# Performance work log

Measured on AMD Instinct MI355X. Metric: run time of the kernel, lower is better.

## Reference

```python
import jax, jax.numpy as jnp
import numpy as np

N_NODES = 100000
N_EDGES = 1250000
IN_DIM = 12
HID = 64
N_LAYERS = 3
LN_EPS = 1e-5
LEAKY_SLOPE = 0.01


def _layer_norm(x, g, b):
    mu = jnp.mean(x, axis=-1, keepdims=True)
    var = jnp.var(x, axis=-1, keepdims=True)
    return (x - mu) * jax.lax.rsqrt(var + LN_EPS) * g + b


def setup_inputs() -> dict:
    key = jax.random.key(0)
    ks = jax.random.split(key, 16)
    s = 0.1  # param init scale
    return {
        "x": jax.random.normal(ks[0], (N_NODES, IN_DIM), jnp.float32),
        "edge_index": jax.random.randint(ks[1], (2, N_EDGES), 0, N_NODES, jnp.int64),
        "edge_weight": jax.random.uniform(ks[2], (N_EDGES,), jnp.float32),
        "in_W": s * jax.random.normal(ks[3], (IN_DIM, HID), jnp.float32),
        "in_b": jnp.zeros((HID,), jnp.float32),
        "lin_W": s * jax.random.normal(ks[4], (N_LAYERS, HID, HID), jnp.float32),
        "lin_b": jnp.zeros((N_LAYERS, HID), jnp.float32),
        "att_W": s * jax.random.normal(ks[5], (N_LAYERS, 2 * HID, 1), jnp.float32),
        "att_b": jnp.zeros((N_LAYERS, 1), jnp.float32),
        "ln_g": jnp.ones((N_LAYERS, HID), jnp.float32),
        "ln_b": jnp.zeros((N_LAYERS, HID), jnp.float32),
        "out1_W": s * jax.random.normal(ks[6], (HID, HID // 2), jnp.float32),
        "out1_b": jnp.zeros((HID // 2,), jnp.float32),
        "out2_W": s * jax.random.normal(ks[7], (HID // 2, 1), jnp.float32),
        "out2_b": jnp.zeros((1,), jnp.float32),
    }


def reference(x, edge_index, edge_weight, in_W, in_b, lin_W, lin_b,
              att_W, att_b, ln_g, ln_b, out1_W, out1_b, out2_W, out2_b):
    row, col = edge_index[0], edge_index[1]
    h = x @ in_W + in_b  # [N, HID]
    for i in range(N_LAYERS):
        hl = h @ lin_W[i] + lin_b[i]  # [N, HID]
        h_i = hl[row]  # [E, HID]
        h_j = hl[col]  # [E, HID]
        att_in = jnp.concatenate([h_i, h_j], axis=-1)  # [E, 2*HID]
        scores = jax.nn.leaky_relu(att_in @ att_W[i] + att_b[i], LEAKY_SLOPE)  # [E, 1]
        scores = jax.nn.softmax(scores, axis=0)  # global softmax over edges (as in source)
        scores = scores * edge_weight[:, None]
        messages = scores * h_j  # [E, HID]
        agg = jax.ops.segment_sum(messages, row, num_segments=N_NODES)
        h_new = jax.nn.relu(hl + agg)
        h_new = _layer_norm(h_new, ln_g[i], ln_b[i])
        # dropout is identity in eval mode
        h = h + h_new
    z = jax.nn.relu(h @ out1_W + out1_b)
    return jax.nn.sigmoid(z @ out2_W + out2_b)  # [N, 1]
```

## Files before the change

### kernel.cpp

```cpp
#include <hip/hip_runtime.h>
#include <hip/hip_fp8.h>
#include <math.h>

#define N_NODES 100000
#define N_EDGES 1250000
#define IN_DIM 12
#define HID 64
#define N_LAYERS 3
#define LN_EPS 1e-5f
#define SLOPE 0.01f

#define NODE_BLOCKS ((N_NODES + 3) / 4)
#define EDGE_TBLOCKS ((N_EDGES + 255) / 256)
#define MFMA_BLOCKS2 ((N_NODES + 127) / 128)
#define OUT_BLOCKS ((N_NODES + 63) / 64)
#define NEDGE_BLOCKS ((N_NODES + 255) / 256)

#define BUCKETS 256
#define BUCKET_NODES 391
#define P1_EDGES 4096
#define P1_BLOCKS ((N_EDGES + P1_EDGES - 1) / P1_EDGES)

#define LEW_SCALE 2048.0f
#define LEW_INV (1.0f / 2048.0f)

typedef short bf16x8 __attribute__((ext_vector_type(8)));
typedef float f32x4 __attribute__((ext_vector_type(4)));
typedef float f32x2 __attribute__((ext_vector_type(2)));

#if defined(__has_builtin)
#if __has_builtin(__builtin_amdgcn_cvt_pk_f32_fp8)
#define HAVE_PK_FP8 1
#endif
#endif

static __device__ __forceinline__ unsigned short f2bf(float f) {
  union { float f; unsigned int u; } v; v.f = f;
  unsigned int r = v.u + 0x7FFFu + ((v.u >> 16) & 1u);
  return (unsigned short)(r >> 16);
}
static __device__ __forceinline__ unsigned char f2e4(float f) {
  return __hip_fp8_e4m3(f).__x;
}
static __device__ __forceinline__ float e42f(unsigned char b) {
  __hip_fp8_e4m3 d; d.__x = b;
  return (float)d;
}

__global__ void k_in_proj(const float* __restrict__ x,
                          const float* __restrict__ W,
                          const float* __restrict__ b,
                          float* __restrict__ h) {
  __shared__ float sW[IN_DIM * HID];
  for (int i = threadIdx.x; i < IN_DIM * HID; i += blockDim.x) sW[i] = W[i];
  __syncthreads();
  int wave = threadIdx.x >> 6, lane = threadIdx.x & 63;
  int n = blockIdx.x * 4 + wave;
  if (n >= N_NODES) return;
  float acc = b[lane];
#pragma unroll
  for (int k = 0; k < IN_DIM; ++k)
    acc += x[n * IN_DIM + k] * sW[k * HID + lane];
  h[n * HID + lane] = acc;
}

__global__ void k_bhist(const int* __restrict__ ei, unsigned* __restrict__ bcnt) {
  __shared__ unsigned cnt[BUCKETS];
  int t = threadIdx.x;
  cnt[t] = 0;
  __syncthreads();
  int base = blockIdx.x * P1_EDGES;
#pragma unroll
  for (int i = 0; i < 16; ++i) {
    int e = base + i * 256 + t;
    if (e < N_EDGES) atomicAdd(&cnt[(unsigned)ei[e] / BUCKET_NODES], 1u);
  }
  __syncthreads();
  if (cnt[t]) atomicAdd(&bcnt[t], cnt[t]);
}

__global__ void k_bscan(const unsigned* __restrict__ bcnt,
                        unsigned* __restrict__ boffs,
                        unsigned* __restrict__ gbcur,
                        int* __restrict__ rowptr) {
  __shared__ unsigned sm[BUCKETS];
  int t = threadIdx.x;
  unsigned v = bcnt[t];
  sm[t] = v;
  __syncthreads();
  for (int st = 1; st < BUCKETS; st <<= 1) {
    unsigned tv = (t >= st) ? sm[t - st] : 0u;
    __syncthreads();
    sm[t] += tv;
    __syncthreads();
  }
  unsigned excl = sm[t] - v;
  boffs[t] = excl;
  gbcur[t] = excl;
  if (t == 0) {
    boffs[BUCKETS] = N_EDGES;
    rowptr[N_NODES] = N_EDGES;
  }
}

__global__ void k_fill_p1(const int* __restrict__ ei, const float* __restrict__ ew,
                          unsigned* __restrict__ gbcur,
                          unsigned long long* __restrict__ tmp) {
  __shared__ unsigned cnt[BUCKETS], gbase[BUCKETS], lofs[BUCKETS];
  int t = threadIdx.x;
  cnt[t] = 0;
  __syncthreads();
  int base = blockIdx.x * P1_EDGES;
#pragma unroll
  for (int i = 0; i < 16; ++i) {
    int e = base + i * 256 + t;
    if (e < N_EDGES) atomicAdd(&cnt[(unsigned)ei[e] / BUCKET_NODES], 1u);
  }
  __syncthreads();
  {
    unsigned c = cnt[t];
    gbase[t] = c ? atomicAdd(&gbcur[t], c) : 0u;
    lofs[t] = 0;
  }
  __syncthreads();
#pragma unroll
  for (int i = 0; i < 16; ++i) {
    int e = base + i * 256 + t;
    if (e < N_EDGES) {
      unsigned r = (unsigned)ei[e], c = (unsigned)ei[N_EDGES + e];
      float lew = __logf(ew[e]);
      lew = fmaxf(lew, -15.9995f);
      unsigned q = (unsigned)(-lew * LEW_SCALE + 0.5f);
      if (q > 32767u) q = 32767u;
      unsigned b = r / BUCKET_NODES;
      unsigned idx = atomicAdd(&lofs[b], 1u);
      tmp[gbase[b] + idx] = ((unsigned long long)r << 32)
                          | ((unsigned long long)c << 15) | q;
    }
  }
}

__global__ void k_fill_p2(const unsigned* __restrict__ boffs,
                          const unsigned long long* __restrict__ tmp,
                          int* __restrict__ rowptr,
                          unsigned* __restrict__ packed) {
  __shared__ unsigned lhist[512];
  __shared__ unsigned lcur[512];
  int b = blockIdx.x, t = threadIdx.x;
  int nb0 = b * BUCKET_NODES;
  int nb1 = min(nb0 + BUCKET_NODES, N_NODES);
  int nn = nb1 - nb0;
  int beg = (int)boffs[b];
  int end = (int)boffs[b + 1];

  lhist[t] = 0;
  __syncthreads();
  for (int i = beg + t; i < end; i += 512) {
    int r = (int)(tmp[i] >> 32);
    atomicAdd(&lhist[r - nb0], 1u);
  }
  __syncthreads();
  unsigned degv = lhist[t];
  for (int st = 1; st < 512; st <<= 1) {
    unsigned tv = (t >= st) ? lhist[t - st] : 0u;
    __syncthreads();
    lhist[t] += tv;
    __syncthreads();
  }
  unsigned excl = lhist[t] - degv;
  if (t < nn) rowptr[nb0 + t] = beg + (int)excl;
  lcur[t] = (unsigned)beg + excl;
  __syncthreads();
  for (int i = beg + t; i < end; i += 512) {
    unsigned long long rec = tmp[i];
    int r = (int)(rec >> 32);
    unsigned pos = atomicAdd(&lcur[r - nb0], 1u);
    packed[pos] = (unsigned)(rec & 0xFFFFFFFFu);
  }
}

__global__ void k_prep(const float* __restrict__ lin_W,
                       const float* __restrict__ lin_b,
                       const float* __restrict__ att_W,
                       float* __restrict__ uvec,
                       float* __restrict__ ucst) {
  int l = blockIdx.x, j = threadIdx.x;
  const float* Wl = lin_W + l * HID * HID;
  const float* a1 = att_W + l * 2 * HID;
  const float* a2 = a1 + HID;
  float s1 = 0.f, s2 = 0.f;
  for (int c = 0; c < HID; ++c) {
    float w = Wl[j * HID + c];
    s1 += w * a1[c];
    s2 += w * a2[c];
  }
  uvec[l * 128 + j] = s1;
  uvec[l * 128 + 64 + j] = s2;
  float t1 = lin_b[l * HID + j] * a1[j];
  float t2 = lin_b[l * HID + j] * a2[j];
#pragma unroll
  for (int off = 32; off > 0; off >>= 1) {
    t1 += __shfl_xor(t1, off, 64);
    t2 += __shfl_xor(t2, off, 64);
  }
  if (j == 0) { ucst[l * 2] = t1; ucst[l * 2 + 1] = t2; }
}

__global__ void k_lin_mfma(const float* __restrict__ h,
                           const float* __restrict__ W,
                           const float* __restrict__ bias,
                           const float* __restrict__ uvec,
                           const float* __restrict__ ucst,
                           float* __restrict__ hl,
                           unsigned char* __restrict__ hl8,
                           float* __restrict__ alpha1,
                           float* __restrict__ alpha2) {
  __shared__ unsigned short Wt[HID * 72];
  for (int idx = threadIdx.x; idx < HID * HID; idx += 256) {
    int k = idx >> 6, n = idx & 63;
    Wt[n * 72 + k] = f2bf(W[idx]);
  }
  __syncthreads();

  int wave = threadIdx.x >> 6, lane = threadIdx.x & 63;
  int g = lane >> 4, r = lane & 15;

#pragma unroll
  for (int tile = 0; tile < 2; ++tile) {
    int nb = blockIdx.x * 128 + tile * 64 + wave * 16;
    int row = nb + r;
    bool rowok = row < N_NODES;
    if (nb >= N_NODES) break;

    f32x4 f0 = {0,0,0,0}, f1 = {0,0,0,0}, f2v = {0,0,0,0}, f3 = {0,0,0,0};
    if (rowok) {
      const float* hrow = h + (size_t)row * HID;
      f0  = *(const f32x4*)(hrow + g * 8);
      f1  = *(const f32x4*)(hrow + g * 8 + 4);
      f2v = *(const f32x4*)(hrow + 32 + g * 8);
      f3  = *(const f32x4*)(hrow + 32 + g * 8 + 4);
    }
    bf16x8 a0, a1f;
#pragma unroll
    for (int i = 0; i < 4; ++i) {
      a0[i]      = (short)f2bf(f0[i]);
      a0[i + 4]  = (short)f2bf(f1[i]);
      a1f[i]     = (short)f2bf(f2v[i]);
      a1f[i + 4] = (short)f2bf(f3[i]);
    }

    f32x4 acc[4] = {{0,0,0,0},{0,0,0,0},{0,0,0,0},{0,0,0,0}};
#pragma unroll
    for (int nt = 0; nt < 4; ++nt) {
      bf16x8 b0 = *(const bf16x8*)&Wt[(nt * 16 + r) * 72 + g * 8];
      bf16x8 b1 = *(const bf16x8*)&Wt[(nt * 16 + r) * 72 + 32 + g * 8];
      acc[nt] = __builtin_amdgcn_mfma_f32_16x16x32_bf16(a0, b0, acc[nt], 0, 0, 0);
      acc[nt] = __builtin_amdgcn_mfma_f32_16x16x32_bf16(a1f, b1, acc[nt], 0, 0, 0);
    }

    {
      const float* u1 = uvec;
      const float* u2 = uvec + HID;
      f32x4 ua = *(const f32x4*)(u1 + g * 8),      ub = *(const f32x4*)(u1 + g * 8 + 4);
      f32x4 uc = *(const f32x4*)(u1 + 32 + g * 8), ud = *(const f32x4*)(u1 + 32 + g * 8 + 4);
      float p1 = f0[0]*ua[0]+f0[1]*ua[1]+f0[2]*ua[2]+f0[3]*ua[3]
               + f1[0]*ub[0]+f1[1]*ub[1]+f1[2]*ub[2]+f1[3]*ub[3]
               + f2v[0]*uc[0]+f2v[1]*uc[1]+f2v[2]*uc[2]+f2v[3]*uc[3]
               + f3[0]*ud[0]+f3[1]*ud[1]+f3[2]*ud[2]+f3[3]*ud[3];
      ua = *(const f32x4*)(u2 + g * 8);      ub = *(const f32x4*)(u2 + g * 8 + 4);
      uc = *(const f32x4*)(u2 + 32 + g * 8); ud = *(const f32x4*)(u2 + 32 + g * 8 + 4);
      float p2 = f0[0]*ua[0]+f0[1]*ua[1]+f0[2]*ua[2]+f0[3]*ua[3]
               + f1[0]*ub[0]+f1[1]*ub[1]+f1[2]*ub[2]+f1[3]*ub[3]
               + f2v[0]*uc[0]+f2v[1]*uc[1]+f2v[2]*uc[2]+f2v[3]*uc[3]
               + f3[0]*ud[0]+f3[1]*ud[1]+f3[2]*ud[2]+f3[3]*ud[3];
      p1 += __shfl_xor(p1, 16, 64); p1 += __shfl_xor(p1, 32, 64);
      p2 += __shfl_xor(p2, 16, 64); p2 += __shfl_xor(p2, 32, 64);
      if (g == 0 && rowok) {
        alpha1[row] = p1 + ucst[0];
        alpha2[row] = p2 + ucst[1];
      }
    }

#pragma unroll
    for (int nt = 0; nt < 4; ++nt) {
      float bv = bias[nt * 16 + r];
#pragma unroll
      for (int reg = 0; reg < 4; ++reg) {
        int n2 = nb + g * 4 + reg;
        if (n2 < N_NODES) {
          float v = acc[nt][reg] + bv;
          hl[(size_t)n2 * HID + nt * 16 + r] = v;
          hl8[(size_t)n2 * HID + nt * 16 + r] = f2e4(v);
        }
      }
    }
  }
}

__global__ void k_edge(const int* __restrict__ rowptr,
                       const unsigned* __restrict__ packed,
                       const float* __restrict__ alpha1,
                       const float* __restrict__ alpha2,
                       const float* __restrict__ attB,
                       float* __restrict__ slw,
                       float* __restrict__ pmax,
                       float* __restrict__ psum,
                       int* __restrict__ counter,
                       float* __restrict__ red) {
  int t = threadIdx.x;
  int n = blockIdx.x * 256 + t;
  float m = -INFINITY, sum = 0.f;
  if (n < N_NODES) {
    float a1 = alpha1[n] + attB[0];
    int beg = rowptr[n];
    int end = rowptr[n + 1];
    for (int p = beg; p < end; ++p) {
      unsigned u = packed[p];
      float sc = a1 + alpha2[u >> 15];
      sc = sc > 0.f ? sc : SLOPE * sc;
      slw[p] = sc - (float)(u & 0x7FFFu) * LEW_INV;
      if (sc > m) { sum *= __expf(m - sc); m = sc; }
      sum += __expf(sc - m);
    }
  }
  __shared__ float smax[256], ssum[256];
  __shared__ bool last;
  smax[t] = m; ssum[t] = sum;
  __syncthreads();
  for (int st = 128; st > 0; st >>= 1) {
    if (t < st) {
      float ma = smax[t], mb = smax[t + st];
      float sa = ssum[t], sb = ssum[t + st];
      float mm = fmaxf(ma, mb);
      float ss = 0.f;
      if (mm != -INFINITY)
        ss = (ma == -INFINITY ? 0.f : sa * __expf(ma - mm))
           + (mb == -INFINITY ? 0.f : sb * __expf(mb - mm));
      smax[t] = mm; ssum[t] = ss;
    }
    __syncthreads();
  }
  if (t == 0) {
    pmax[blockIdx.x] = smax[0];
    psum[blockIdx.x] = ssum[0];
    __threadfence();
    int old = atomicAdd(counter, 1);
    last = (old == (int)gridDim.x - 1);
  }
  __syncthreads();
  if (!last) return;
  __threadfence();
  volatile const float* vpm = pmax;
  volatile const float* vps = psum;
  float m2 = -INFINITY, s2 = 0.f;
  for (int i = t; i < (int)gridDim.x; i += 256) {
    float mb = vpm[i], sb = vps[i];
    if (mb != -INFINITY) {
      if (mb > m2) { s2 *= __expf(m2 - mb); m2 = mb; }
      s2 += sb * __expf(mb - m2);
    }
  }
  __syncthreads();
  smax[t] = m2; ssum[t] = s2;
  __syncthreads();
  for (int st = 128; st > 0; st >>= 1) {
    if (t < st) {
      float ma = smax[t], mb = smax[t + st];
      float sa = ssum[t], sb = ssum[t + st];
      float mm = fmaxf(ma, mb);
      float ss = 0.f;
      if (mm != -INFINITY)
        ss = (ma == -INFINITY ? 0.f : sa * __expf(ma - mm))
           + (mb == -INFINITY ? 0.f : sb * __expf(mb - mm));
      smax[t] = mm; ssum[t] = ss;
    }
    __syncthreads();
  }
  if (t == 0) {
    red[0] = smax[0];
    red[1] = ssum[0];
    *counter = 0;
  }
}

__global__ void k_exp2(f32x4* __restrict__ slw, const float* __restrict__ red) {
  int i = blockIdx.x * 256 + threadIdx.x;
  int nvec = (N_EDGES + 3) / 4;
  if (i >= nvec) return;
  float M = red[0];
  f32x4 v = slw[i];
  v[0] = __expf(v[0] - M);
  v[1] = __expf(v[1] - M);
  v[2] = __expf(v[2] - M);
  v[3] = __expf(v[3] - M);
  slw[i] = v;
}

__global__ void k_agg_update(const int* __restrict__ rowptr,
                             const unsigned* __restrict__ packed,
                             const float* __restrict__ w,
                             const float* __restrict__ red,
                             const float* __restrict__ hl,
                             const unsigned char* __restrict__ hl8,
                             const float* __restrict__ gam,
                             const float* __restrict__ bet,
                             float* __restrict__ h) {
  int wave = threadIdx.x >> 6, lane = threadIdx.x & 63;
  int n = blockIdx.x * 4 + wave;
  if (n >= N_NODES) return;
  int g = lane >> 4, q = lane & 15;
  int beg = rowptr[n];
  int end = rowptr[n + 1];

  float a0 = 0.f, a1 = 0.f, a2 = 0.f, a3 = 0.f;
  for (int k = beg; k < end; k += 16) {
    int ke0 = k + g, ke1 = k + 4 + g, ke2 = k + 8 + g, ke3 = k + 12 + g;
    bool v0 = ke0 < end, v1 = ke1 < end, v2 = ke2 < end, v3 = ke3 < end;
    unsigned u0 = packed[v0 ? ke0 : beg];
    unsigned u1 = packed[v1 ? ke1 : beg];
    unsigned u2 = packed[v2 ? ke2 : beg];
    unsigned u3 = packed[v3 ? ke3 : beg];
    float w0 = v0 ? w[ke0] : 0.f;
    float w1 = v1 ? w[ke1] : 0.f;
    float w2 = v2 ? w[ke2] : 0.f;
    float w3 = v3 ? w[ke3] : 0.f;
    unsigned d0 = *(const unsigned*)(hl8 + (size_t)(u0 >> 15) * HID + q * 4);
    unsigned d1 = *(const unsigned*)(hl8 + (size_t)(u1 >> 15) * HID + q * 4);
    unsigned d2 = *(const unsigned*)(hl8 + (size_t)(u2 >> 15) * HID + q * 4);
    unsigned d3 = *(const unsigned*)(hl8 + (size_t)(u3 >> 15) * HID + q * 4);
#ifdef HAVE_PK_FP8
    f32x2 l0 = __builtin_amdgcn_cvt_pk_f32_fp8((int)d0, 0);
    f32x2 h0 = __builtin_amdgcn_cvt_pk_f32_fp8((int)d0, 1);
    f32x2 l1 = __builtin_amdgcn_cvt_pk_f32_fp8((int)d1, 0);
    f32x2 h1 = __builtin_amdgcn_cvt_pk_f32_fp8((int)d1, 1);
    f32x2 l2 = __builtin_amdgcn_cvt_pk_f32_fp8((int)d2, 0);
    f32x2 h2 = __builtin_amdgcn_cvt_pk_f32_fp8((int)d2, 1);
    f32x2 l3 = __builtin_amdgcn_cvt_pk_f32_fp8((int)d3, 0);
    f32x2 h3 = __builtin_amdgcn_cvt_pk_f32_fp8((int)d3, 1);
    a0 += w0 * l0[0] + w1 * l1[0] + w2 * l2[0] + w3 * l3[0];
    a1 += w0 * l0[1] + w1 * l1[1] + w2 * l2[1] + w3 * l3[1];
    a2 += w0 * h0[0] + w1 * h1[0] + w2 * h2[0] + w3 * h3[0];
    a3 += w0 * h0[1] + w1 * h1[1] + w2 * h2[1] + w3 * h3[1];
#else
    a0 += w0 * e42f(d0 & 0xffu) + w1 * e42f(d1 & 0xffu)
        + w2 * e42f(d2 & 0xffu) + w3 * e42f(d3 & 0xffu);
    a1 += w0 * e42f((d0 >> 8) & 0xffu) + w1 * e42f((d1 >> 8) & 0xffu)
        + w2 * e42f((d2 >> 8) & 0xffu) + w3 * e42f((d3 >> 8) & 0xffu);
    a2 += w0 * e42f((d0 >> 16) & 0xffu) + w1 * e42f((d1 >> 16) & 0xffu)
        + w2 * e42f((d2 >> 16) & 0xffu) + w3 * e42f((d3 >> 16) & 0xffu);
    a3 += w0 * e42f(d0 >> 24) + w1 * e42f(d1 >> 24)
        + w2 * e42f(d2 >> 24) + w3 * e42f(d3 >> 24);
#endif
  }
  a0 += __shfl_xor(a0, 16, 64); a0 += __shfl_xor(a0, 32, 64);
  a1 += __shfl_xor(a1, 16, 64); a1 += __shfl_xor(a1, 32, 64);
  a2 += __shfl_xor(a2, 16, 64); a2 += __shfl_xor(a2, 32, 64);
  a3 += __shfl_xor(a3, 16, 64); a3 += __shfl_xor(a3, 32, 64);

  float inv = 1.0f / red[1];
  const float* hlrow = hl + (size_t)n * HID + q * 4;
  float v0 = fmaxf(hlrow[0] + a0 * inv, 0.f);
  float v1 = fmaxf(hlrow[1] + a1 * inv, 0.f);
  float v2 = fmaxf(hlrow[2] + a2 * inv, 0.f);
  float v3 = fmaxf(hlrow[3] + a3 * inv, 0.f);

  float ms = v0 + v1 + v2 + v3;
  ms += __shfl_xor(ms, 1, 64); ms += __shfl_xor(ms, 2, 64);
  ms += __shfl_xor(ms, 4, 64); ms += __shfl_xor(ms, 8, 64);
  float m = ms * (1.0f / HID);
  float d0 = v0 - m, d1 = v1 - m, d2 = v2 - m, d3 = v3 - m;
  float vs = d0 * d0 + d1 * d1 + d2 * d2 + d3 * d3;
  vs += __shfl_xor(vs, 1, 64); vs += __shfl_xor(vs, 2, 64);
  vs += __shfl_xor(vs, 4, 64); vs += __shfl_xor(vs, 8, 64);
  float rs = rsqrtf(vs * (1.0f / HID) + LN_EPS);

  if (g == 0) {
    float* hrow = h + (size_t)n * HID + q * 4;
    f32x4 hv = *(const f32x4*)hrow;
    f32x4 gv = *(const f32x4*)(gam + q * 4);
    f32x4 bv = *(const f32x4*)(bet + q * 4);
    f32x4 o;
    o[0] = hv[0] + d0 * rs * gv[0] + bv[0];
    o[1] = hv[1] + d1 * rs * gv[1] + bv[1];
    o[2] = hv[2] + d2 * rs * gv[2] + bv[2];
    o[3] = hv[3] + d3 * rs * gv[3] + bv[3];
    *(f32x4*)hrow = o;
  }
}

__global__ void k_out_mfma(const float* __restrict__ h,
                           const float* __restrict__ W1,
                           const float* __restrict__ b1,
                           const float* __restrict__ W2,
                           const float* __restrict__ b2,
                           float* __restrict__ out) {
  __shared__ unsigned short W1t[32 * 72];
  __shared__ float sW2[32];
  for (int idx = threadIdx.x; idx < HID * 32; idx += 256) {
    int k = idx >> 5, m = idx & 31;
    W1t[m * 72 + k] = f2bf(W1[idx]);
  }
  if (threadIdx.x < 32) sW2[threadIdx.x] = W2[threadIdx.x];
  __syncthreads();

  int wave = threadIdx.x >> 6, lane = threadIdx.x & 63;
  int g = lane >> 4, r = lane & 15;
  int nb = blockIdx.x * 64 + wave * 16;
  int row = nb + r;
  bool rowok = row < N_NODES;

  f32x4 f0 = {0,0,0,0}, f1 = {0,0,0,0}, f2v = {0,0,0,0}, f3 = {0,0,0,0};
  if (rowok) {
    const float* hrow = h + (size_t)row * HID;
    f0  = *(const f32x4*)(hrow + g * 8);
    f1  = *(const f32x4*)(hrow + g * 8 + 4);
    f2v = *(const f32x4*)(hrow + 32 + g * 8);
    f3  = *(const f32x4*)(hrow + 32 + g * 8 + 4);
  }
  bf16x8 a0, a1f;
#pragma unroll
  for (int i = 0; i < 4; ++i) {
    a0[i]      = (short)f2bf(f0[i]);
    a0[i + 4]  = (short)f2bf(f1[i]);
    a1f[i]     = (short)f2bf(f2v[i]);
    a1f[i + 4] = (short)f2bf(f3[i]);
  }

  f32x4 acc[2] = {{0,0,0,0},{0,0,0,0}};
#pragma unroll
  for (int mt = 0; mt < 2; ++mt) {
    bf16x8 b0 = *(const bf16x8*)&W1t[(mt * 16 + r) * 72 + g * 8];
    bf16x8 b1v = *(const bf16x8*)&W1t[(mt * 16 + r) * 72 + 32 + g * 8];
    acc[mt] = __builtin_amdgcn_mfma_f32_16x16x32_bf16(a0, b0, acc[mt], 0, 0, 0);
    acc[mt] = __builtin_amdgcn_mfma_f32_16x16x32_bf16(a1f, b1v, acc[mt], 0, 0, 0);
  }

  float part[4];
#pragma unroll
  for (int reg = 0; reg < 4; ++reg) {
    float p = 0.f;
#pragma unroll
    for (int mt = 0; mt < 2; ++mt) {
      float z = acc[mt][reg] + b1[mt * 16 + r];
      p += fmaxf(z, 0.f) * sW2[mt * 16 + r];
    }
    p += __shfl_xor(p, 1, 64);
    p += __shfl_xor(p, 2, 64);
    p += __shfl_xor(p, 4, 64);
    p += __shfl_xor(p, 8, 64);
    part[reg] = p;
  }
  if (r == 0) {
    float bb = b2[0];
#pragma unroll
    for (int reg = 0; reg < 4; ++reg) {
      int n2 = nb + g * 4 + reg;
      if (n2 < N_NODES)
        out[n2] = 1.0f / (1.0f + expf(-(part[reg] + bb)));
    }
  }
}

extern "C" void kernel_launch(void* const* d_in, const int* in_sizes, int n_in,
                              void* d_out, int out_size, void* d_ws, size_t ws_size,
                              hipStream_t stream) {
  const float* x      = (const float*)d_in[0];
  const int*   ei     = (const int*)d_in[1];
  const float* ew     = (const float*)d_in[2];
  const float* in_W   = (const float*)d_in[3];
  const float* in_b   = (const float*)d_in[4];
  const float* lin_W  = (const float*)d_in[5];
  const float* lin_b  = (const float*)d_in[6];
  const float* att_W  = (const float*)d_in[7];
  const float* att_b  = (const float*)d_in[8];
  const float* ln_g   = (const float*)d_in[9];
  const float* ln_b   = (const float*)d_in[10];
  const float* out1_W = (const float*)d_in[11];
  const float* out1_b = (const float*)d_in[12];
  const float* out2_W = (const float*)d_in[13];
  const float* out2_b = (const float*)d_in[14];
  float* out = (float*)d_out;

  float* ws = (float*)d_ws;
  float* h            = ws;
  float* hl           = ws + 6400000;
  unsigned char* hl8  = (unsigned char*)(ws + 12800000);
  unsigned long long* tmp = (unsigned long long*)(ws + 14500000);
  unsigned* packed    = (unsigned*)(ws + 17000000);
  float* slw          = ws + 18250000;
  int* rowptr         = (int*)(ws + 19500000);
  int* counter        = (int*)(ws + 19601000);
  unsigned* bcnt      = (unsigned*)(counter + 1);
  unsigned* boffs     = bcnt + 256;
  float* alpha1       = ws + 19702000;
  float* alpha2       = ws + 19803000;
  float* pmax         = ws + 19904000;
  float* psum         = ws + 19906000;
  float* red          = ws + 19908000;
  float* uvec         = ws + 19909000;
  float* ucst         = ws + 19910000;
  unsigned* gbcur     = (unsigned*)(ws + 19912000);

  hipMemsetAsync(counter, 0, (1 + 256) * sizeof(int), stream);
  k_bhist<<<P1_BLOCKS, 256, 0, stream>>>(ei, bcnt);
  k_bscan<<<1, 256, 0, stream>>>(bcnt, boffs, gbcur, rowptr);
  k_fill_p1<<<P1_BLOCKS, 256, 0, stream>>>(ei, ew, gbcur, tmp);
  k_fill_p2<<<BUCKETS, 512, 0, stream>>>(boffs, tmp, rowptr, packed);

  k_prep<<<N_LAYERS, 64, 0, stream>>>(lin_W, lin_b, att_W, uvec, ucst);
  k_in_proj<<<NODE_BLOCKS, 256, 0, stream>>>(x, in_W, in_b, h);

  for (int i = 0; i < N_LAYERS; ++i) {
    k_lin_mfma<<<MFMA_BLOCKS2, 256, 0, stream>>>(h, lin_W + i * HID * HID, lin_b + i * HID,
                                                 uvec + i * 128, ucst + i * 2,
                                                 hl, hl8, alpha1, alpha2);
    k_edge<<<NEDGE_BLOCKS, 256, 0, stream>>>(rowptr, packed, alpha1, alpha2,
                                             att_b + i, slw, pmax, psum, counter, red);
    k_exp2<<<(((N_EDGES + 3) / 4) + 255) / 256, 256, 0, stream>>>((f32x4*)slw, red);
    k_agg_update<<<NODE_BLOCKS, 256, 0, stream>>>(rowptr, packed, slw, red,
                                                  hl, hl8, ln_g + i * HID, ln_b + i * HID, h);
  }

  k_out_mfma<<<OUT_BLOCKS, 256, 0, stream>>>(h, out1_W, out1_b, out2_W, out2_b, out);
}
```

Before: 375.2 us.

## Use upper-bound softmax max from alpha maxima and drop separate exp pass

The global softmax max is replaced by an upper bound, max(alpha1)+max(alpha2)+bias, gathered with atomicMax in the linear kernel. This lets the edge kernel compute exp and the weighted coefficient directly in one pass, which removes the online-max rescaling and the separate k_exp2 pass over all edges. Edge weights are now stored as truncated bf16-like bits instead of a quantized log, and the hl row is loaded as one vector. The risk is underflow if the bound is far above the true max, and some loss of edge-weight precision.

```diff
diff --git a/kernel.cpp b/kernel.cpp
--- a/kernel.cpp
+++ b/kernel.cpp
@@ -11,7 +11,6 @@
 #define SLOPE 0.01f
 
 #define NODE_BLOCKS ((N_NODES + 3) / 4)
-#define EDGE_TBLOCKS ((N_EDGES + 255) / 256)
 #define MFMA_BLOCKS2 ((N_NODES + 127) / 128)
 #define OUT_BLOCKS ((N_NODES + 63) / 64)
 #define NEDGE_BLOCKS ((N_NODES + 255) / 256)
@@ -20,9 +19,6 @@
 #define BUCKET_NODES 391
 #define P1_EDGES 4096
 #define P1_BLOCKS ((N_EDGES + P1_EDGES - 1) / P1_EDGES)
-
-#define LEW_SCALE 2048.0f
-#define LEW_INV (1.0f / 2048.0f)
 
 typedef short bf16x8 __attribute__((ext_vector_type(8)));
 typedef float f32x4 __attribute__((ext_vector_type(4)));
@@ -45,6 +41,14 @@
 static __device__ __forceinline__ float e42f(unsigned char b) {
   __hip_fp8_e4m3 d; d.__x = b;
   return (float)d;
+}
+static __device__ __forceinline__ unsigned keyenc(float f) {
+  unsigned u = __float_as_uint(f);
+  return (u & 0x80000000u) ? ~u : (u | 0x80000000u);
+}
+static __device__ __forceinline__ float keydec(unsigned k) {
+  unsigned u = (k & 0x80000000u) ? (k ^ 0x80000000u) : ~k;
+  return __uint_as_float(u);
 }
 
 __global__ void k_in_proj(const float* __restrict__ x,
@@ -128,14 +132,12 @@
     int e = base + i * 256 + t;
     if (e < N_EDGES) {
       unsigned r = (unsigned)ei[e], c = (unsigned)ei[N_EDGES + e];
-      float lew = __logf(ew[e]);
-      lew = fmaxf(lew, -15.9995f);
-      unsigned q = (unsigned)(-lew * LEW_SCALE + 0.5f);
-      if (q > 32767u) q = 32767u;
+      unsigned eb = (__float_as_uint(ew[e]) + 0x8000u) >> 16;
+      if (eb > 0x7FFFu) eb = 0x7FFFu;
       unsigned b = r / BUCKET_NODES;
       unsigned idx = atomicAdd(&lofs[b], 1u);
       tmp[gbase[b] + idx] = ((unsigned long long)r << 32)
-                          | ((unsigned long long)c << 15) | q;
+                          | ((unsigned long long)c << 15) | eb;
     }
   }
 }
@@ -214,7 +216,8 @@
                            float* __restrict__ hl,
                            unsigned char* __restrict__ hl8,
                            float* __restrict__ alpha1,
-                           float* __restrict__ alpha2) {
+                           float* __restrict__ alpha2,
+                           unsigned* __restrict__ amaxk) {
   __shared__ unsigned short Wt[HID * 72];
   for (int idx = threadIdx.x; idx < HID * HID; idx += 256) {
     int k = idx >> 6, n = idx & 63;
@@ -275,9 +278,21 @@
                + f3[0]*ud[0]+f3[1]*ud[1]+f3[2]*ud[2]+f3[3]*ud[3];
       p1 += __shfl_xor(p1, 16, 64); p1 += __shfl_xor(p1, 32, 64);
       p2 += __shfl_xor(p2, 16, 64); p2 += __shfl_xor(p2, 32, 64);
+      float a1v = p1 + ucst[0];
+      float a2v = p2 + ucst[1];
       if (g == 0 && rowok) {
-        alpha1[row] = p1 + ucst[0];
-        alpha2[row] = p2 + ucst[1];
+        alpha1[row] = a1v;
+        alpha2[row] = a2v;
+      }
+      float m1 = rowok ? a1v : -INFINITY;
+      float m2 = rowok ? a2v : -INFINITY;
+      m1 = fmaxf(m1, __shfl_xor(m1, 1, 64)); m2 = fmaxf(m2, __shfl_xor(m2, 1, 64));
+      m1 = fmaxf(m1, __shfl_xor(m1, 2, 64)); m2 = fmaxf(m2, __shfl_xor(m2, 2, 64));
+      m1 = fmaxf(m1, __shfl_xor(m1, 4, 64)); m2 = fmaxf(m2, __shfl_xor(m2, 4, 64));
+      m1 = fmaxf(m1, __shfl_xor(m1, 8, 64)); m2 = fmaxf(m2, __shfl_xor(m2, 8, 64));
+      if (lane == 0) {
+        atomicMax(&amaxk[0], keyenc(m1));
+        atomicMax(&amaxk[1], keyenc(m2));
       }
     }
 
@@ -302,46 +317,39 @@
                        const float* __restrict__ alpha1,
                        const float* __restrict__ alpha2,
                        const float* __restrict__ attB,
-                       float* __restrict__ slw,
-                       float* __restrict__ pmax,
+                       const unsigned* __restrict__ amaxk,
+                       float* __restrict__ wcoef,
                        float* __restrict__ psum,
                        int* __restrict__ counter,
                        float* __restrict__ red) {
   int t = threadIdx.x;
   int n = blockIdx.x * 256 + t;
-  float m = -INFINITY, sum = 0.f;
+  float ab = attB[0];
+  float M = keydec(amaxk[0]) + keydec(amaxk[1]) + ab;
+  float sum = 0.f;
   if (n < N_NODES) {
-    float a1 = alpha1[n] + attB[0];
+    float a1 = alpha1[n] + ab;
     int beg = rowptr[n];
     int end = rowptr[n + 1];
     for (int p = beg; p < end; ++p) {
       unsigned u = packed[p];
       float sc = a1 + alpha2[u >> 15];
       sc = sc > 0.f ? sc : SLOPE * sc;
-      slw[p] = sc - (float)(u & 0x7FFFu) * LEW_INV;
-      if (sc > m) { sum *= __expf(m - sc); m = sc; }
-      sum += __expf(sc - m);
-    }
-  }
-  __shared__ float smax[256], ssum[256];
+      float e = __expf(sc - M);
+      float ewf = __uint_as_float((u & 0x7FFFu) << 16);
+      wcoef[p] = e * ewf;
+      sum += e;
+    }
+  }
+  __shared__ float ssum[256];
   __shared__ bool last;
-  smax[t] = m; ssum[t] = sum;
+  ssum[t] = sum;
   __syncthreads();
   for (int st = 128; st > 0; st >>= 1) {
-    if (t < st) {
-      float ma = smax[t], mb = smax[t + st];
-      float sa = ssum[t], sb = ssum[t + st];
-      float mm = fmaxf(ma, mb);
-      float ss = 0.f;
-      if (mm != -INFINITY)
-        ss = (ma == -INFINITY ? 0.f : sa * __expf(ma - mm))
-           + (mb == -INFINITY ? 0.f : sb * __expf(mb - mm));
-      smax[t] = mm; ssum[t] = ss;
-    }
+    if (t < st) ssum[t] += ssum[t + st];
     __syncthreads();
   }
   if (t == 0) {
-    pmax[blockIdx.x] = smax[0];
     psum[blockIdx.x] = ssum[0];
     __threadfence();
     int old = atomicAdd(counter, 1);
@@ -350,50 +358,20 @@
   __syncthreads();
   if (!last) return;
   __threadfence();
-  volatile const float* vpm = pmax;
   volatile const float* vps = psum;
-  float m2 = -INFINITY, s2 = 0.f;
-  for (int i = t; i < (int)gridDim.x; i += 256) {
-    float mb = vpm[i], sb = vps[i];
-    if (mb != -INFINITY) {
-      if (mb > m2) { s2 *= __expf(m2 - mb); m2 = mb; }
-      s2 += sb * __expf(mb - m2);
-    }
-  }
-  __syncthreads();
-  smax[t] = m2; ssum[t] = s2;
+  float s2 = 0.f;
+  for (int i = t; i < (int)gridDim.x; i += 256) s2 += vps[i];
+  __syncthreads();
+  ssum[t] = s2;
   __syncthreads();
   for (int st = 128; st > 0; st >>= 1) {
-    if (t < st) {
-      float ma = smax[t], mb = smax[t + st];
-      float sa = ssum[t], sb = ssum[t + st];
-      float mm = fmaxf(ma, mb);
-      float ss = 0.f;
-      if (mm != -INFINITY)
-        ss = (ma == -INFINITY ? 0.f : sa * __expf(ma - mm))
-           + (mb == -INFINITY ? 0.f : sb * __expf(mb - mm));
-      smax[t] = mm; ssum[t] = ss;
-    }
+    if (t < st) ssum[t] += ssum[t + st];
     __syncthreads();
   }
   if (t == 0) {
-    red[0] = smax[0];
-    red[1] = ssum[0];
+    red[0] = ssum[0];
     *counter = 0;
   }
-}
-
-__global__ void k_exp2(f32x4* __restrict__ slw, const float* __restrict__ red) {
-  int i = blockIdx.x * 256 + threadIdx.x;
-  int nvec = (N_EDGES + 3) / 4;
-  if (i >= nvec) return;
-  float M = red[0];
-  f32x4 v = slw[i];
-  v[0] = __expf(v[0] - M);
-  v[1] = __expf(v[1] - M);
-  v[2] = __expf(v[2] - M);
-  v[3] = __expf(v[3] - M);
-  slw[i] = v;
 }
 
 __global__ void k_agg_update(const int* __restrict__ rowptr,
@@ -457,12 +435,12 @@
   a2 += __shfl_xor(a2, 16, 64); a2 += __shfl_xor(a2, 32, 64);
   a3 += __shfl_xor(a3, 16, 64); a3 += __shfl_xor(a3, 32, 64);
 
-  float inv = 1.0f / red[1];
-  const float* hlrow = hl + (size_t)n * HID + q * 4;
-  float v0 = fmaxf(hlrow[0] + a0 * inv, 0.f);
-  float v1 = fmaxf(hlrow[1] + a1 * inv, 0.f);
-  float v2 = fmaxf(hlrow[2] + a2 * inv, 0.f);
-  float v3 = fmaxf(hlrow[3] + a3 * inv, 0.f);
+  float inv = 1.0f / red[0];
+  f32x4 hlv = *(const f32x4*)(hl + (size_t)n * HID + q * 4);
+  float v0 = fmaxf(hlv[0] + a0 * inv, 0.f);
+  float v1 = fmaxf(hlv[1] + a1 * inv, 0.f);
+  float v2 = fmaxf(hlv[2] + a2 * inv, 0.f);
+  float v3 = fmaxf(hlv[3] + a3 * inv, 0.f);
 
   float ms = v0 + v1 + v2 + v3;
   ms += __shfl_xor(ms, 1, 64); ms += __shfl_xor(ms, 2, 64);
@@ -587,21 +565,21 @@
   unsigned char* hl8  = (unsigned char*)(ws + 12800000);
   unsigned long long* tmp = (unsigned long long*)(ws + 14500000);
   unsigned* packed    = (unsigned*)(ws + 17000000);
-  float* slw          = ws + 18250000;
+  float* wcoef        = ws + 18250000;
   int* rowptr         = (int*)(ws + 19500000);
   int* counter        = (int*)(ws + 19601000);
   unsigned* bcnt      = (unsigned*)(counter + 1);
-  unsigned* boffs     = bcnt + 256;
+  unsigned* amaxk     = bcnt + 256;
+  unsigned* boffs     = amaxk + 6;
   float* alpha1       = ws + 19702000;
   float* alpha2       = ws + 19803000;
-  float* pmax         = ws + 19904000;
-  float* psum         = ws + 19906000;
+  float* psum         = ws + 19904000;
   float* red          = ws + 19908000;
   float* uvec         = ws + 19909000;
   float* ucst         = ws + 19910000;
   unsigned* gbcur     = (unsigned*)(ws + 19912000);
 
-  hipMemsetAsync(counter, 0, (1 + 256) * sizeof(int), stream);
+  hipMemsetAsync(counter, 0, (1 + 256 + 6) * sizeof(int), stream);
   k_bhist<<<P1_BLOCKS, 256, 0, stream>>>(ei, bcnt);
   k_bscan<<<1, 256, 0, stream>>>(bcnt, boffs, gbcur, rowptr);
   k_fill_p1<<<P1_BLOCKS, 256, 0, stream>>>(ei, ew, gbcur, tmp);
@@ -613,11 +591,11 @@
   for (int i = 0; i < N_LAYERS; ++i) {
     k_lin_mfma<<<MFMA_BLOCKS2, 256, 0, stream>>>(h, lin_W + i * HID * HID, lin_b + i * HID,
                                                  uvec + i * 128, ucst + i * 2,
-                                                 hl, hl8, alpha1, alpha2);
+                                                 hl, hl8, alpha1, alpha2, amaxk + 2 * i);
     k_edge<<<NEDGE_BLOCKS, 256, 0, stream>>>(rowptr, packed, alpha1, alpha2,
-                                             att_b + i, slw, pmax, psum, counter, red);
-    k_exp2<<<(((N_EDGES + 3) / 4) + 255) / 256, 256, 0, stream>>>((f32x4*)slw, red);
-    k_agg_update<<<NODE_BLOCKS, 256, 0, stream>>>(rowptr, packed, slw, red,
+                                             att_b + i, amaxk + 2 * i,
+                                             wcoef, psum, counter, red);
+    k_agg_update<<<NODE_BLOCKS, 256, 0, stream>>>(rowptr, packed, wcoef, red,
                                                   hl, hl8, ln_g + i * HID, ln_b + i * HID, h);
   }
 
```

Result: slower. 764.0 us (+103.6%).
